# Performance work log

Hardware: AMD Instinct MI355X
Metric: run time of the kernel (lower is better)

Reference implementation:

```python
import jax, jax.numpy as jnp
import numpy as np

B, CIN, HALF, H, W = 4, 3, 32, 512, 512
K_MODE, PAD_MODE, N_LEVELS = 11, 5, 17  # 11x11 mode window, reflect pad 5, round(x*255/16) in 0..16
SLOPE, EPS = 0.01, 1e-5


def _leaky(x):
    return jnp.where(x > 0, x, SLOPE * x)


def _bn(x, g, b):
    # BatchNorm2d in training mode: batch statistics over (B,H,W), biased var
    m = x.mean(axis=(0, 2, 3), keepdims=True)
    v = x.var(axis=(0, 2, 3), keepdims=True)
    return (x - m) * jax.lax.rsqrt(v + EPS) * g[None, :, None, None] + b[None, :, None, None]


def _mode_pool(x):
    # quantize to 17 discrete levels, then sliding-window histogram mode (fused
    # equivalent of unfold + torch.mode; argmax first-hit == smallest tied value)
    k = jnp.clip(jnp.round(x * (255.0 / 16.0)), 0, N_LEVELS - 1).astype(jnp.int32)
    kp = jnp.pad(k, ((0, 0), (0, 0), (PAD_MODE, PAD_MODE), (PAD_MODE, PAD_MODE)), mode='reflect')
    onehot = (kp[..., None] == jnp.arange(N_LEVELS, dtype=jnp.int32)).astype(jnp.float32)
    counts = jax.lax.reduce_window(onehot, 0.0, jax.lax.add,
                                   (1, 1, K_MODE, K_MODE, 1), (1, 1, 1, 1, 1), 'VALID')
    mode_k = jnp.argmax(counts, axis=-1)  # [B,C,H,W]
    return mode_k.astype(jnp.float32) * (16.0 / 256.0)


def _nearest(x, Ho, Wo):
    # torch interpolate(mode='nearest'): src = floor(dst * in/out)
    hi, wi = x.shape[2], x.shape[3]
    ri = (jnp.arange(Ho) * hi) // Ho
    ci = (jnp.arange(Wo) * wi) // Wo
    return x[:, :, ri][:, :, :, ci]


def _forward(x, w1, b1, w2, b2, bn1_g, bn1_b, w3, b3, bn2_g, bn2_b,
             k_down, k_w, bnw_g, bnw_b, k_h, bnh_g, bnh_b):
    xm = _mode_pool(x)  # [B,CIN,H,W]
    # prepare: 1x1 conv -> LeakyReLU -> 1x1 conv -> BN -> LeakyReLU -> depthwise 1x1 -> BN -> LeakyReLU
    h = _leaky(jnp.einsum('bchw,oc->bohw', xm, w1) + b1[None, :, None, None])
    h = jnp.einsum('bchw,oc->bohw', h, w2) + b2[None, :, None, None]
    h = _leaky(_bn(h, bn1_g, bn1_b))
    h = h * w3[None, :, None, None] + b3[None, :, None, None]  # groups=half 1x1 conv
    h = _leaky(_bn(h, bn2_g, bn2_b))
    Bs, half, Ho, Wo = h.shape
    score = jnp.zeros((Bs, 2 * half, Ho, Wo), jnp.float32)
    d = h
    while min(d.shape[2], d.shape[3]) >= 3:  # static pyramid: 512->171->57->19->7->3->1
        d = jax.lax.conv_general_dilated(d, k_down, (3, 3), ((1, 1), (1, 1)),
                                         dimension_numbers=('NCHW', 'OIHW', 'NCHW'),
                                         feature_group_count=half)
        z = _nearest(d, Ho, Wo)
        wbr = _leaky(_bn(z * k_w[None, :, None, None], bnw_g, bnw_b))  # width branch (SharedConv k=1, no bias)
        hbr = _leaky(_bn(z * k_h[None, :, None, None], bnh_g, bnh_b))  # height branch
        # stack(dim=1).reshape => width channels first, then height channels
        score = score + jnp.concatenate([wbr, hbr], axis=1)
    return score


def setup_inputs():
    key = jax.random.key(0)
    ks = jax.random.split(key, 8)
    x = jax.random.uniform(ks[0], (B, CIN, H, W), dtype=jnp.float32)
    s1, s2 = 1.0 / np.sqrt(CIN), 1.0 / np.sqrt(2 * CIN)
    return {
        'x': x,
        'w1': jax.random.uniform(ks[1], (2 * CIN, CIN), jnp.float32, -s1, s1),
        'b1': jax.random.uniform(ks[2], (2 * CIN,), jnp.float32, -s1, s1),
        'w2': jax.random.uniform(ks[3], (HALF, 2 * CIN), jnp.float32, -s2, s2),
        'b2': jax.random.uniform(ks[4], (HALF,), jnp.float32, -s2, s2),
        'bn1_g': jnp.ones((HALF,), jnp.float32),
        'bn1_b': jnp.zeros((HALF,), jnp.float32),
        'w3': jax.random.uniform(ks[5], (HALF,), jnp.float32, -1.0, 1.0),
        'b3': jax.random.uniform(ks[6], (HALF,), jnp.float32, -1.0, 1.0),
        'bn2_g': jnp.ones((HALF,), jnp.float32),
        'bn2_b': jnp.zeros((HALF,), jnp.float32),
        'k_down': jnp.full((HALF, 1, 3, 3), 0.5, jnp.float32),  # SharedConv init
        'k_w': jnp.full((HALF,), 0.5, jnp.float32),
        'bnw_g': jnp.ones((HALF,), jnp.float32),
        'bnw_b': jnp.zeros((HALF,), jnp.float32),
        'k_h': jnp.full((HALF,), 0.5, jnp.float32),
        'bnh_g': jnp.ones((HALF,), jnp.float32),
        'bnh_b': jnp.zeros((HALF,), jnp.float32),
    }


def reference(x, w1, b1, w2, b2, bn1_g, bn1_b, w3, b3, bn2_g, bn2_b,
              k_down, k_w, bnw_g, bnw_b, k_h, bnh_g, bnh_b):
    return _forward(x, w1, b1, w2, b2, bn1_g, bn1_b, w3, b3, bn2_g, bn2_b,
                    k_down, k_w, bnw_g, bnw_b, k_h, bnh_g, bnh_b)
```

## Files before the change

kernel.cpp:

```cpp
#include <hip/hip_runtime.h>

#define HH 512
#define WW 512
#define HW 262144
#define NPIX 1048576
#define NPIXF 1048576.0f

typedef float f4 __attribute__((ext_vector_type(4)));

__device__ __forceinline__ float leaky(float v) { return v > 0.f ? v : 0.01f * v; }

__device__ __forceinline__ float repw(int i, int s) {
    return (float)(((i + 1) * 512 + s - 1) / s - (i * 512 + s - 1) / s);
}

__device__ __forceinline__ void hins(unsigned long long& h0, unsigned long long& h1,
                                     unsigned& c16, int val) {
    unsigned long long inc = 1ull << ((val & 7) * 8);
    h0 += (val < 8) ? inc : 0;
    h1 += (val >= 8 && val < 16) ? inc : 0;
    c16 += (unsigned)(val >> 4);
}
__device__ __forceinline__ void hrem(unsigned long long& h0, unsigned long long& h1,
                                     unsigned& c16, int val) {
    unsigned long long inc = 1ull << ((val & 7) * 8);
    h0 -= (val < 8) ? inc : 0;
    h1 -= (val >= 8 && val < 16) ? inc : 0;
    c16 -= (unsigned)(val >> 4);
}

__global__ __launch_bounds__(256) void mode_kernel(const float* __restrict__ x,
                                                   unsigned char* __restrict__ modeq,
                                                   const float* __restrict__ w1,
                                                   const float* __restrict__ b1,
                                                   unsigned* __restrict__ partial,
                                                   float* __restrict__ mpart) {
    __shared__ unsigned char q[26 * 272];
    __shared__ unsigned ch[2][267 * 5];
    __shared__ unsigned lh[4913];
    __shared__ float mred[27][4];
    const int t = threadIdx.x;
    for (int i = t; i < 4913; i += 256) lh[i] = 0;
    const int tc0 = blockIdx.x * 256;
    const int tr0 = blockIdx.y * 16;
    const int bb = blockIdx.z;
    unsigned rp[3][4];
    for (int p = 0; p < 3; ++p) {
        const float* xp = x + (size_t)(bb * 3 + p) * HW;
        for (int idx = t; idx < 26 * 266; idx += 256) {
            int r = idx / 266;
            int cc = idx - r * 266;
            int gr = tr0 + r - 5; gr = gr < 0 ? -gr : (gr > 511 ? 1022 - gr : gr);
            int gc = tc0 + cc - 5; gc = gc < 0 ? -gc : (gc > 511 ? 1022 - gc : gc);
            float v = rintf(xp[gr * WW + gc] * 15.9375f);
            v = fminf(fmaxf(v, 0.f), 16.f);
            q[r * 272 + cc] = (unsigned char)(int)v;
        }
        unsigned long long A0 = 0, A1 = 0; unsigned A2 = 0;
        unsigned long long B0 = 0, B1 = 0; unsigned B2 = 0;
        unsigned wkw[4] = {0u, 0u, 0u, 0u};
        __syncthreads();
        for (int r = 0; r < 16; ++r) {
            if (r == 0) {
                #pragma unroll
                for (int v = 0; v < 11; ++v) {
                    hins(A0, A1, A2, q[v * 272 + t]);
                    if (t < 10) hins(B0, B1, B2, q[v * 272 + 256 + t]);
                }
            } else {
                hrem(A0, A1, A2, q[(r - 1) * 272 + t]);
                hins(A0, A1, A2, q[(r + 10) * 272 + t]);
                if (t < 10) {
                    hrem(B0, B1, B2, q[(r - 1) * 272 + 256 + t]);
                    hins(B0, B1, B2, q[(r + 10) * 272 + 256 + t]);
                }
            }
            unsigned* cb = ch[r & 1];
            cb[t * 5 + 0] = (unsigned)A0;
            cb[t * 5 + 1] = (unsigned)(A0 >> 32);
            cb[t * 5 + 2] = (unsigned)A1;
            cb[t * 5 + 3] = (unsigned)(A1 >> 32);
            cb[t * 5 + 4] = A2;
            if (t < 10) {
                cb[(256 + t) * 5 + 0] = (unsigned)B0;
                cb[(256 + t) * 5 + 1] = (unsigned)(B0 >> 32);
                cb[(256 + t) * 5 + 2] = (unsigned)B1;
                cb[(256 + t) * 5 + 3] = (unsigned)(B1 >> 32);
                cb[(256 + t) * 5 + 4] = B2;
            }
            __syncthreads();
            unsigned long long H0 = 0, H1 = 0; unsigned C = 0;
            #pragma unroll
            for (int v = 0; v < 11; ++v) {
                const unsigned* pk = &cb[(t + v) * 5];
                H0 += (unsigned long long)pk[0] | ((unsigned long long)pk[1] << 32);
                H1 += (unsigned long long)pk[2] | ((unsigned long long)pk[3] << 32);
                C += pk[4];
            }
            unsigned m = 0;
            #pragma unroll
            for (int i = 0; i < 8; ++i) {
                unsigned cnt = (unsigned)(H0 >> (8 * i)) & 0xFFu;
                unsigned val = (cnt << 8) | (unsigned)(16 - i);
                m = m > val ? m : val;
            }
            #pragma unroll
            for (int i = 8; i < 16; ++i) {
                unsigned cnt = (unsigned)(H1 >> (8 * (i - 8))) & 0xFFu;
                unsigned val = (cnt << 8) | (unsigned)(16 - i);
                m = m > val ? m : val;
            }
            unsigned val16 = (C << 8);
            m = m > val16 ? m : val16;
            int k = 16 - (int)(m & 0xFFu);
            wkw[r >> 2] |= (unsigned)k << ((r & 3) * 8);
            modeq[(size_t)(bb * 3 + p) * HW + (size_t)(tr0 + r) * WW + tc0 + t] = (unsigned char)k;
        }
        rp[p][0] = wkw[0]; rp[p][1] = wkw[1]; rp[p][2] = wkw[2]; rp[p][3] = wkw[3];
    }
    #pragma unroll
    for (int r = 0; r < 16; ++r) {
        int sh = (r & 3) * 8;
        int k0 = (rp[0][r >> 2] >> sh) & 0xFF;
        int k1 = (rp[1][r >> 2] >> sh) & 0xFF;
        int k2 = (rp[2][r >> 2] >> sh) & 0xFF;
        atomicAdd(&lh[k0 + 17 * k1 + 289 * k2], 1u);
    }
    __syncthreads();
    const int blk = blockIdx.x + 2 * (blockIdx.y + 32 * blockIdx.z);
    for (int i = t; i < 4913; i += 256) partial[i * 256 + blk] = lh[i];
    float w1r[18], b1r[6];
    #pragma unroll
    for (int k = 0; k < 18; ++k) w1r[k] = w1[k];
    #pragma unroll
    for (int o = 0; o < 6; ++o) b1r[o] = b1[o];
    float M[27];
    #pragma unroll
    for (int i = 0; i < 27; ++i) M[i] = 0.f;
    for (int bin = t; bin < 4913; bin += 256) {
        float cnt = (float)lh[bin];
        int k0 = bin % 17;
        int r = bin / 17;
        int k1 = r % 17;
        int k2 = r / 17;
        float xm0 = k0 * 0.0625f, xm1 = k1 * 0.0625f, xm2 = k2 * 0.0625f;
        float t1[6];
        #pragma unroll
        for (int o = 0; o < 6; ++o)
            t1[o] = leaky(xm0 * w1r[o * 3] + xm1 * w1r[o * 3 + 1] + xm2 * w1r[o * 3 + 2] + b1r[o]);
        #pragma unroll
        for (int o = 0; o < 6; ++o) M[o] += cnt * t1[o];
        int ii = 6;
        #pragma unroll
        for (int j = 0; j < 6; ++j)
            #pragma unroll
            for (int k = j; k < 6; ++k) { M[ii] += cnt * t1[j] * t1[k]; ++ii; }
    }
    int wv = t >> 6;
    #pragma unroll
    for (int i = 0; i < 27; ++i) {
        float v = M[i];
        #pragma unroll
        for (int off = 32; off >= 1; off >>= 1) v += __shfl_xor(v, off);
        if ((t & 63) == 0) mred[i][wv] = v;
    }
    __syncthreads();
    if (t < 27)
        mpart[blk * 27 + t] = mred[t][0] + mred[t][1] + mred[t][2] + mred[t][3];
}

__global__ __launch_bounds__(1024) void solveA_kernel(const float* __restrict__ mpart,
                                                      const float* __restrict__ w2,
                                                      const float* __restrict__ b2,
                                                      const float* __restrict__ g1,
                                                      const float* __restrict__ bb1,
                                                      float* __restrict__ p1) {
    __shared__ float red[32][32];
    __shared__ float mom[27];
    int t = threadIdx.x;
    int i = t & 31, g = t >> 5;
    float s = 0.f;
    if (i < 27) {
        #pragma unroll
        for (int j = 0; j < 8; ++j) s += mpart[(g + 32 * j) * 27 + i];
    }
    red[g][i] = s;
    __syncthreads();
    if (t < 27) {
        float v = 0.f;
        #pragma unroll
        for (int gg = 0; gg < 32; ++gg) v += red[gg][t];
        mom[t] = v;
    }
    __syncthreads();
    if (t < 32) {
        int c = t;
        float w2r[6];
        #pragma unroll
        for (int k = 0; k < 6; ++k) w2r[k] = w2[c * 6 + k];
        float b2c = b2[c];
        float wm1 = 0.f;
        #pragma unroll
        for (int k = 0; k < 6; ++k) wm1 += w2r[k] * mom[k];
        float q = 0.f;
        int ii = 6;
        #pragma unroll
        for (int j = 0; j < 6; ++j)
            #pragma unroll
            for (int k = j; k < 6; ++k) {
                float f = w2r[j] * w2r[k] * mom[ii];
                q += (j == k) ? f : 2.f * f;
                ++ii;
            }
        float mean = b2c + wm1 / NPIXF;
        float ex2 = b2c * b2c + 2.f * b2c * (wm1 / NPIXF) + q / NPIXF;
        float var = ex2 - mean * mean;
        float a = g1[c] * rsqrtf(var + 1e-5f);
        p1[c] = a;
        p1[32 + c] = bb1[c] - mean * a;
    }
}

__global__ __launch_bounds__(256) void solveB_kernel(const unsigned* __restrict__ partial,
                                                     const float* __restrict__ w1,
                                                     const float* __restrict__ b1,
                                                     const float* __restrict__ w2,
                                                     const float* __restrict__ b2,
                                                     const float* __restrict__ p1,
                                                     float* __restrict__ tpart) {
    __shared__ float rs[8][32], rq[8][32];
    int c = threadIdx.x & 31;
    int sub = threadIdx.x >> 5;
    float w1r[18], b1r[6];
    #pragma unroll
    for (int k = 0; k < 18; ++k) w1r[k] = w1[k];
    #pragma unroll
    for (int o = 0; o < 6; ++o) b1r[o] = b1[o];
    float w2r[6];
    #pragma unroll
    for (int k = 0; k < 6; ++k) w2r[k] = w2[c * 6 + k];
    float b2c = b2[c];
    float a1 = p1[c], c1 = p1[32 + c];
    float sm = 0.f, sq = 0.f;
    for (int bin = blockIdx.x + 32 * sub; bin < 4913; bin += 256) {
        unsigned cs = 0;
        const unsigned* pb = partial + (size_t)bin * 256;
        #pragma unroll
        for (int j = 0; j < 8; ++j) cs += pb[c + 32 * j];
        #pragma unroll
        for (int off = 16; off >= 1; off >>= 1) cs += __shfl_xor((int)cs, off);
        float cnt = (float)cs;
        int k0 = bin % 17;
        int r = bin / 17;
        int k1 = r % 17;
        int k2 = r / 17;
        float xm0 = k0 * 0.0625f, xm1 = k1 * 0.0625f, xm2 = k2 * 0.0625f;
        float t1[6];
        #pragma unroll
        for (int o = 0; o < 6; ++o)
            t1[o] = leaky(xm0 * w1r[o * 3] + xm1 * w1r[o * 3 + 1] + xm2 * w1r[o * 3 + 2] + b1r[o]);
        float h2 = b2c;
        #pragma unroll
        for (int k = 0; k < 6; ++k) h2 += w2r[k] * t1[k];
        float t = leaky(a1 * h2 + c1);
        sm += cnt * t;
        sq += cnt * t * t;
    }
    rs[sub][c] = sm; rq[sub][c] = sq;
    __syncthreads();
    if (threadIdx.x < 32) {
        float s = 0.f, qq = 0.f;
        #pragma unroll
        for (int g = 0; g < 8; ++g) { s += rs[g][threadIdx.x]; qq += rq[g][threadIdx.x]; }
        tpart[blockIdx.x * 64 + threadIdx.x] = s;
        tpart[blockIdx.x * 64 + 32 + threadIdx.x] = qq;
    }
}

__global__ void fin2_kernel(const float* __restrict__ tpart, const float* __restrict__ w3,
                            const float* __restrict__ b3, const float* __restrict__ g,
                            const float* __restrict__ bb, float* __restrict__ p2) {
    int c = threadIdx.x;
    float s = 0.f, qq = 0.f;
    #pragma unroll
    for (int k = 0; k < 32; ++k) { s += tpart[k * 64 + c]; qq += tpart[k * 64 + 32 + c]; }
    float mt = s / NPIXF;
    float vt = qq / NPIXF - mt * mt;
    float m2 = w3[c] * mt + b3[c];
    float v2 = w3[c] * w3[c] * vt;
    float a = g[c] * rsqrtf(v2 + 1e-5f);
    p2[c] = a;
    p2[32 + c] = bb[c] - m2 * a;
}

__global__ __launch_bounds__(64) void d1_kernel(const unsigned char* __restrict__ modeq,
                                                const float* __restrict__ w1,
                                                const float* __restrict__ b1,
                                                const float* __restrict__ w2,
                                                const float* __restrict__ b2,
                                                const float* __restrict__ w3,
                                                const float* __restrict__ b3,
                                                const float* __restrict__ p1,
                                                const float* __restrict__ p2,
                                                const float* __restrict__ kd,
                                                float* __restrict__ d1) {
    int j = blockIdx.x * 64 + threadIdx.x;
    if (j >= 171) return;
    int i = blockIdx.y;
    int b = blockIdx.z;
    float acc[32];
    #pragma unroll
    for (int c = 0; c < 32; ++c) acc[c] = 0.f;
    const unsigned char* mp = modeq + (size_t)b * 3 * HW;
    #pragma unroll
    for (int u = 0; u < 3; ++u) {
        int r = 3 * i - 1 + u;
        if (r < 0 || r > 511) continue;
        #pragma unroll
        for (int v = 0; v < 3; ++v) {
            int col = 3 * j - 1 + v;
            if (col < 0 || col > 511) continue;
            int off = r * WW + col;
            float xm0 = mp[off] * 0.0625f, xm1 = mp[off + HW] * 0.0625f, xm2 = mp[off + 2 * HW] * 0.0625f;
            float t1[6];
            #pragma unroll
            for (int o = 0; o < 6; ++o)
                t1[o] = leaky(xm0 * w1[o * 3] + xm1 * w1[o * 3 + 1] + xm2 * w1[o * 3 + 2] + b1[o]);
            #pragma unroll
            for (int c = 0; c < 32; ++c) {
                float h2 = b2[c];
                #pragma unroll
                for (int k = 0; k < 6; ++k) h2 += w2[c * 6 + k] * t1[k];
                float t = leaky(h2 * p1[c] + p1[32 + c]);
                float uu = t * w3[c] + b3[c];
                float hv = leaky(uu * p2[c] + p2[32 + c]);
                acc[c] += hv * kd[c * 9 + u * 3 + v];
            }
        }
    }
    size_t base = ((size_t)(b * 32) * 171 + i) * 171 + j;
    #pragma unroll
    for (int c = 0; c < 32; ++c) d1[base + (size_t)c * 29241] = acc[c];
}

__device__ __forceinline__ void red_store(float sm, float sq, float* rsc, float* ps) {
    #pragma unroll
    for (int off = 32; off >= 1; off >>= 1) {
        sm += __shfl_xor(sm, off);
        sq += __shfl_xor(sq, off);
    }
    __syncthreads();
    int wv = threadIdx.x >> 6;
    if ((threadIdx.x & 63) == 0) { rsc[wv] = sm; rsc[8 + wv] = sq; }
    __syncthreads();
    if (threadIdx.x == 0) {
        ps[0] = rsc[0] + rsc[1] + rsc[2] + rsc[3];
        ps[1] = rsc[8] + rsc[9] + rsc[10] + rsc[11];
    }
}

__device__ __forceinline__ void lvl(const float* src, int sin, float* dstL,
                                    float* dstG, int sout, const float* kreg,
                                    float* rsc, float* ps) {
    float sm = 0.f, sq = 0.f;
    int n = sout * sout;
    for (int i = threadIdx.x; i < n; i += 256) {
        int oi = i / sout, oj = i - oi * sout;
        float acc = 0.f;
        #pragma unroll
        for (int u = 0; u < 3; ++u) {
            int r = 3 * oi - 1 + u;
            if ((unsigned)r >= (unsigned)sin) continue;
            #pragma unroll
            for (int v = 0; v < 3; ++v) {
                int cc = 3 * oj - 1 + v;
                if ((unsigned)cc >= (unsigned)sin) continue;
                acc += src[r * sin + cc] * kreg[u * 3 + v];
            }
        }
        dstG[i] = acc;
        if (dstL) dstL[i] = acc;
        float w = repw(oi, sout) * repw(oj, sout);
        sm += w * acc;
        sq += w * acc * acc;
    }
    red_store(sm, sq, rsc, ps);
}

__global__ __launch_bounds__(256) void pyramid_kernel(const float* __restrict__ d1,
                                                      float* __restrict__ d2,
                                                      float* __restrict__ d3,
                                                      float* __restrict__ d4,
                                                      float* __restrict__ d5,
                                                      float* __restrict__ d6,
                                                      const float* __restrict__ kd,
                                                      float* __restrict__ pstats) {
    __shared__ float buf2[3249];
    __shared__ float buf3[361];
    __shared__ float buf4[49];
    __shared__ float buf5[9];
    __shared__ float rsc[16];
    int bc = blockIdx.x;
    int c = bc & 31;
    float kreg[9];
    #pragma unroll
    for (int qq = 0; qq < 9; ++qq) kreg[qq] = kd[c * 9 + qq];
    float* ps = pstats + (size_t)bc * 12;
    const float* s1 = d1 + (size_t)bc * 29241;
    float sm = 0.f, sq = 0.f;
    for (int i = threadIdx.x; i < 29241; i += 256) {
        int oi = i / 171, oj = i - oi * 171;
        float w = repw(oi, 171) * repw(oj, 171);
        float v = s1[i];
        sm += w * v;
        sq += w * v * v;
    }
    red_store(sm, sq, rsc, ps + 0);
    lvl(s1, 171, buf2, d2 + (size_t)bc * 3249, 57, kreg, rsc, ps + 2);
    lvl(buf2, 57, buf3, d3 + (size_t)bc * 361, 19, kreg, rsc, ps + 4);
    lvl(buf3, 19, buf4, d4 + (size_t)bc * 49, 7, kreg, rsc, ps + 6);
    lvl(buf4, 7, buf5, d5 + (size_t)bc * 9, 3, kreg, rsc, ps + 8);
    lvl(buf5, 3, nullptr, d6 + bc, 1, kreg, rsc, ps + 10);
}

__global__ void fin3_kernel(const float* __restrict__ pstats, const float* __restrict__ kw,
                            const float* __restrict__ gw, const float* __restrict__ bw,
                            const float* __restrict__ kh, const float* __restrict__ gh,
                            const float* __restrict__ bh, float* __restrict__ lp) {
    int t = threadIdx.x;
    if (t >= 192) return;
    int l = t >> 5, c = t & 31;
    float sm = 0.f, sq = 0.f;
    #pragma unroll
    for (int b = 0; b < 4; ++b) {
        const float* ps = pstats + (size_t)(b * 32 + c) * 12 + 2 * l;
        sm += ps[0];
        sq += ps[1];
    }
    float mz = sm / NPIXF;
    float vz = sq / NPIXF - mz * mz;
    float kwc = kw[c];
    float aw = gw[c] * rsqrtf(kwc * kwc * vz + 1e-5f);
    float khc = kh[c];
    float ah = gh[c] * rsqrtf(khc * khc * vz + 1e-5f);
    float* o = lp + (size_t)(l * 32 + c) * 4;
    o[0] = kwc * aw;
    o[1] = bw[c] - kwc * mz * aw;
    o[2] = khc * ah;
    o[3] = bh[c] - khc * mz * ah;
}

__global__ __launch_bounds__(256) void final_kernel(const float* __restrict__ d1,
                                                    const float* __restrict__ d2,
                                                    const float* __restrict__ d3,
                                                    const float* __restrict__ d4,
                                                    const float* __restrict__ d5,
                                                    const float* __restrict__ d6,
                                                    const float* __restrict__ lp,
                                                    float* __restrict__ out) {
    int idx = blockIdx.x * 256 + threadIdx.x;
    int w4 = (idx & 127) << 2;
    int h = (idx >> 7) & 511;
    int c = (idx >> 16) & 31;
    int b = idx >> 21;
    const float* ds[6] = {d1, d2, d3, d4, d5, d6};
    const int ss[6] = {171, 57, 19, 7, 3, 1};
    float accw[4] = {0.f, 0.f, 0.f, 0.f};
    float acch[4] = {0.f, 0.f, 0.f, 0.f};
    #pragma unroll
    for (int l = 0; l < 6; ++l) {
        int s = ss[l];
        int sh = (h * s) >> 9;
        const float* base = ds[l] + ((size_t)(b * 32 + c) * s + sh) * s;
        const float* a = lp + (size_t)(l * 32 + c) * 4;
        float a0 = a[0], a1 = a[1], a2 = a[2], a3 = a[3];
        #pragma unroll
        for (int k = 0; k < 4; ++k) {
            int sw = ((w4 + k) * s) >> 9;
            float val = base[sw];
            accw[k] += leaky(val * a0 + a1);
            acch[k] += leaky(val * a2 + a3);
        }
    }
    size_t o = (((size_t)(b * 64 + c)) << 18) + ((size_t)h << 9) + w4;
    f4 vw = {accw[0], accw[1], accw[2], accw[3]};
    f4 vh = {acch[0], acch[1], acch[2], acch[3]};
    __builtin_nontemporal_store(vw, (f4*)(out + o));
    __builtin_nontemporal_store(vh, (f4*)(out + o + (((size_t)32) << 18)));
}

extern "C" void kernel_launch(void* const* d_in, const int* in_sizes, int n_in,
                              void* d_out, int out_size, void* d_ws, size_t ws_size,
                              hipStream_t stream) {
    const float* x     = (const float*)d_in[0];
    const float* w1    = (const float*)d_in[1];
    const float* b1    = (const float*)d_in[2];
    const float* w2    = (const float*)d_in[3];
    const float* b2    = (const float*)d_in[4];
    const float* bn1g  = (const float*)d_in[5];
    const float* bn1b  = (const float*)d_in[6];
    const float* w3    = (const float*)d_in[7];
    const float* b3    = (const float*)d_in[8];
    const float* bn2g  = (const float*)d_in[9];
    const float* bn2b  = (const float*)d_in[10];
    const float* kd    = (const float*)d_in[11];
    const float* kw    = (const float*)d_in[12];
    const float* bnwg  = (const float*)d_in[13];
    const float* bnwb  = (const float*)d_in[14];
    const float* kh    = (const float*)d_in[15];
    const float* bnhg  = (const float*)d_in[16];
    const float* bnhb  = (const float*)d_in[17];
    float* out = (float*)d_out;

    char* ws = (char*)d_ws;
    unsigned char* modeq = (unsigned char*)ws;
    float* mpart  = (float*)(ws + 3145728);
    float* tpart  = (float*)(ws + 3145728 + 27648);
    float* pstats = (float*)(ws + 3145728 + 27648 + 8192);
    float* p1 = (float*)(ws + 3187712);
    float* p2 = p1 + 64;
    float* lp = p2 + 64;
    unsigned* partial = (unsigned*)(ws + 3191296);
    float* d1 = (float*)(ws + 3191296 + 5030912);
    float* d2 = d1 + 3742848;
    float* d3 = d2 + 415872;
    float* d4 = d3 + 46208;
    float* d5 = d4 + 6272;
    float* d6 = d5 + 1152;

    mode_kernel<<<dim3(2, 32, 4), 256, 0, stream>>>(x, modeq, w1, b1, partial, mpart);
    solveA_kernel<<<1, 1024, 0, stream>>>(mpart, w2, b2, bn1g, bn1b, p1);
    solveB_kernel<<<32, 256, 0, stream>>>(partial, w1, b1, w2, b2, p1, tpart);
    fin2_kernel<<<1, 32, 0, stream>>>(tpart, w3, b3, bn2g, bn2b, p2);
    d1_kernel<<<dim3(3, 171, 4), 64, 0, stream>>>(modeq, w1, b1, w2, b2, w3, b3, p1, p2, kd, d1);
    pyramid_kernel<<<128, 256, 0, stream>>>(d1, d2, d3, d4, d5, d6, kd, pstats);
    fin3_kernel<<<1, 192, 0, stream>>>(pstats, kw, bnwg, bnwb, kh, bnhg, bnhb, lp);
    final_kernel<<<32768, 256, 0, stream>>>(d1, d2, d3, d4, d5, d6, lp, out);
}
```

Baseline: 504.4 us.

## Split mode pooling per plane, move joint histogram to separate kernel, fuse tiny solvers

The mode kernel now runs one block per (tile, plane) across 12 planes instead of looping over 3 channels inside each block, giving three times more blocks. The joint 3-channel histogram and moment accumulation move into a new hist_kernel that rereads the quantized mode bytes. solveA is folded into solveB, with every block recomputing the BN1 parameters, and fin3 is folded into final_kernel, with each block recomputing its per-channel coefficients. This removes two launches and gives the mode pass more parallelism, at the cost of an extra read of modeq and redundant small computations.

```diff
diff --git a/kernel.cpp b/kernel.cpp
--- a/kernel.cpp
+++ b/kernel.cpp
@@ -30,105 +30,114 @@
 }
 
 __global__ __launch_bounds__(256) void mode_kernel(const float* __restrict__ x,
-                                                   unsigned char* __restrict__ modeq,
+                                                   unsigned char* __restrict__ modeq) {
+    __shared__ unsigned char q[26 * 272];
+    __shared__ unsigned ch[2][267 * 5];
+    const int plane = blockIdx.z;
+    const int tc0 = blockIdx.x * 256;
+    const int tr0 = blockIdx.y * 16;
+    const float* xp = x + (size_t)plane * HW;
+    for (int idx = threadIdx.x; idx < 26 * 266; idx += 256) {
+        int r = idx / 266;
+        int cc = idx - r * 266;
+        int gr = tr0 + r - 5; gr = gr < 0 ? -gr : (gr > 511 ? 1022 - gr : gr);
+        int gc = tc0 + cc - 5; gc = gc < 0 ? -gc : (gc > 511 ? 1022 - gc : gc);
+        float v = rintf(xp[gr * WW + gc] * 15.9375f);
+        v = fminf(fmaxf(v, 0.f), 16.f);
+        q[r * 272 + cc] = (unsigned char)(int)v;
+    }
+    const int t = threadIdx.x;
+    unsigned long long A0 = 0, A1 = 0; unsigned A2 = 0;
+    unsigned long long B0 = 0, B1 = 0; unsigned B2 = 0;
+    __syncthreads();
+    for (int r = 0; r < 16; ++r) {
+        if (r == 0) {
+            #pragma unroll
+            for (int v = 0; v < 11; ++v) {
+                hins(A0, A1, A2, q[v * 272 + t]);
+                if (t < 10) hins(B0, B1, B2, q[v * 272 + 256 + t]);
+            }
+        } else {
+            hrem(A0, A1, A2, q[(r - 1) * 272 + t]);
+            hins(A0, A1, A2, q[(r + 10) * 272 + t]);
+            if (t < 10) {
+                hrem(B0, B1, B2, q[(r - 1) * 272 + 256 + t]);
+                hins(B0, B1, B2, q[(r + 10) * 272 + 256 + t]);
+            }
+        }
+        unsigned* cb = ch[r & 1];
+        cb[t * 5 + 0] = (unsigned)A0;
+        cb[t * 5 + 1] = (unsigned)(A0 >> 32);
+        cb[t * 5 + 2] = (unsigned)A1;
+        cb[t * 5 + 3] = (unsigned)(A1 >> 32);
+        cb[t * 5 + 4] = A2;
+        if (t < 10) {
+            cb[(256 + t) * 5 + 0] = (unsigned)B0;
+            cb[(256 + t) * 5 + 1] = (unsigned)(B0 >> 32);
+            cb[(256 + t) * 5 + 2] = (unsigned)B1;
+            cb[(256 + t) * 5 + 3] = (unsigned)(B1 >> 32);
+            cb[(256 + t) * 5 + 4] = B2;
+        }
+        __syncthreads();
+        unsigned long long H0 = 0, H1 = 0; unsigned C = 0;
+        #pragma unroll
+        for (int v = 0; v < 11; ++v) {
+            const unsigned* p = &cb[(t + v) * 5];
+            H0 += (unsigned long long)p[0] | ((unsigned long long)p[1] << 32);
+            H1 += (unsigned long long)p[2] | ((unsigned long long)p[3] << 32);
+            C += p[4];
+        }
+        unsigned m = 0;
+        #pragma unroll
+        for (int i = 0; i < 8; ++i) {
+            unsigned cnt = (unsigned)(H0 >> (8 * i)) & 0xFFu;
+            unsigned val = (cnt << 8) | (unsigned)(16 - i);
+            m = m > val ? m : val;
+        }
+        #pragma unroll
+        for (int i = 8; i < 16; ++i) {
+            unsigned cnt = (unsigned)(H1 >> (8 * (i - 8))) & 0xFFu;
+            unsigned val = (cnt << 8) | (unsigned)(16 - i);
+            m = m > val ? m : val;
+        }
+        unsigned val16 = (C << 8);
+        m = m > val16 ? m : val16;
+        int k = 16 - (int)(m & 0xFFu);
+        modeq[(size_t)plane * HW + (size_t)(tr0 + r) * WW + tc0 + t] = (unsigned char)k;
+    }
+}
+
+__global__ __launch_bounds__(256) void hist_kernel(const unsigned char* __restrict__ modeq,
                                                    const float* __restrict__ w1,
                                                    const float* __restrict__ b1,
                                                    unsigned* __restrict__ partial,
                                                    float* __restrict__ mpart) {
-    __shared__ unsigned char q[26 * 272];
-    __shared__ unsigned ch[2][267 * 5];
     __shared__ unsigned lh[4913];
     __shared__ float mred[27][4];
-    const int t = threadIdx.x;
-    for (int i = t; i < 4913; i += 256) lh[i] = 0;
-    const int tc0 = blockIdx.x * 256;
-    const int tr0 = blockIdx.y * 16;
-    const int bb = blockIdx.z;
-    unsigned rp[3][4];
-    for (int p = 0; p < 3; ++p) {
-        const float* xp = x + (size_t)(bb * 3 + p) * HW;
-        for (int idx = t; idx < 26 * 266; idx += 256) {
-            int r = idx / 266;
-            int cc = idx - r * 266;
-            int gr = tr0 + r - 5; gr = gr < 0 ? -gr : (gr > 511 ? 1022 - gr : gr);
-            int gc = tc0 + cc - 5; gc = gc < 0 ? -gc : (gc > 511 ? 1022 - gc : gc);
-            float v = rintf(xp[gr * WW + gc] * 15.9375f);
-            v = fminf(fmaxf(v, 0.f), 16.f);
-            q[r * 272 + cc] = (unsigned char)(int)v;
-        }
-        unsigned long long A0 = 0, A1 = 0; unsigned A2 = 0;
-        unsigned long long B0 = 0, B1 = 0; unsigned B2 = 0;
-        unsigned wkw[4] = {0u, 0u, 0u, 0u};
-        __syncthreads();
-        for (int r = 0; r < 16; ++r) {
-            if (r == 0) {
-                #pragma unroll
-                for (int v = 0; v < 11; ++v) {
-                    hins(A0, A1, A2, q[v * 272 + t]);
-                    if (t < 10) hins(B0, B1, B2, q[v * 272 + 256 + t]);
-                }
-            } else {
-                hrem(A0, A1, A2, q[(r - 1) * 272 + t]);
-                hins(A0, A1, A2, q[(r + 10) * 272 + t]);
-                if (t < 10) {
-                    hrem(B0, B1, B2, q[(r - 1) * 272 + 256 + t]);
-                    hins(B0, B1, B2, q[(r + 10) * 272 + 256 + t]);
-                }
-            }
-            unsigned* cb = ch[r & 1];
-            cb[t * 5 + 0] = (unsigned)A0;
-            cb[t * 5 + 1] = (unsigned)(A0 >> 32);
-            cb[t * 5 + 2] = (unsigned)A1;
-            cb[t * 5 + 3] = (unsigned)(A1 >> 32);
-            cb[t * 5 + 4] = A2;
-            if (t < 10) {
-                cb[(256 + t) * 5 + 0] = (unsigned)B0;
-                cb[(256 + t) * 5 + 1] = (unsigned)(B0 >> 32);
-                cb[(256 + t) * 5 + 2] = (unsigned)B1;
-                cb[(256 + t) * 5 + 3] = (unsigned)(B1 >> 32);
-                cb[(256 + t) * 5 + 4] = B2;
-            }
-            __syncthreads();
-            unsigned long long H0 = 0, H1 = 0; unsigned C = 0;
-            #pragma unroll
-            for (int v = 0; v < 11; ++v) {
-                const unsigned* pk = &cb[(t + v) * 5];
-                H0 += (unsigned long long)pk[0] | ((unsigned long long)pk[1] << 32);
-                H1 += (unsigned long long)pk[2] | ((unsigned long long)pk[3] << 32);
-                C += pk[4];
-            }
-            unsigned m = 0;
-            #pragma unroll
-            for (int i = 0; i < 8; ++i) {
-                unsigned cnt = (unsigned)(H0 >> (8 * i)) & 0xFFu;
-                unsigned val = (cnt << 8) | (unsigned)(16 - i);
-                m = m > val ? m : val;
-            }
-            #pragma unroll
-            for (int i = 8; i < 16; ++i) {
-                unsigned cnt = (unsigned)(H1 >> (8 * (i - 8))) & 0xFFu;
-                unsigned val = (cnt << 8) | (unsigned)(16 - i);
-                m = m > val ? m : val;
-            }
-            unsigned val16 = (C << 8);
-            m = m > val16 ? m : val16;
-            int k = 16 - (int)(m & 0xFFu);
-            wkw[r >> 2] |= (unsigned)k << ((r & 3) * 8);
-            modeq[(size_t)(bb * 3 + p) * HW + (size_t)(tr0 + r) * WW + tc0 + t] = (unsigned char)k;
-        }
-        rp[p][0] = wkw[0]; rp[p][1] = wkw[1]; rp[p][2] = wkw[2]; rp[p][3] = wkw[3];
-    }
-    #pragma unroll
-    for (int r = 0; r < 16; ++r) {
-        int sh = (r & 3) * 8;
-        int k0 = (rp[0][r >> 2] >> sh) & 0xFF;
-        int k1 = (rp[1][r >> 2] >> sh) & 0xFF;
-        int k2 = (rp[2][r >> 2] >> sh) & 0xFF;
-        atomicAdd(&lh[k0 + 17 * k1 + 289 * k2], 1u);
-    }
-    __syncthreads();
-    const int blk = blockIdx.x + 2 * (blockIdx.y + 32 * blockIdx.z);
-    for (int i = t; i < 4913; i += 256) partial[i * 256 + blk] = lh[i];
+    for (int i = threadIdx.x; i < 4913; i += 256) lh[i] = 0;
+    __syncthreads();
+    int base = blockIdx.x * 8192;
+    int b = base >> 18;
+    int hw0 = base & (HW - 1);
+    const unsigned char* mp = modeq + (size_t)b * 3 * HW;
+    #pragma unroll
+    for (int j = 0; j < 8; ++j) {
+        int g = threadIdx.x + 256 * j;
+        int hw = hw0 + g * 4;
+        unsigned u0 = *(const unsigned*)(mp + hw);
+        unsigned u1 = *(const unsigned*)(mp + hw + HW);
+        unsigned u2 = *(const unsigned*)(mp + hw + 2 * HW);
+        #pragma unroll
+        for (int k = 0; k < 4; ++k) {
+            int k0 = (u0 >> (8 * k)) & 0xFF;
+            int k1 = (u1 >> (8 * k)) & 0xFF;
+            int k2 = (u2 >> (8 * k)) & 0xFF;
+            atomicAdd(&lh[k0 + 17 * k1 + 289 * k2], 1u);
+        }
+    }
+    __syncthreads();
+    unsigned* pp = partial + blockIdx.x * 4913;
+    for (int i = threadIdx.x; i < 4913; i += 256) pp[i] = lh[i];
     float w1r[18], b1r[6];
     #pragma unroll
     for (int k = 0; k < 18; ++k) w1r[k] = w1[k];
@@ -137,7 +146,7 @@
     float M[27];
     #pragma unroll
     for (int i = 0; i < 27; ++i) M[i] = 0.f;
-    for (int bin = t; bin < 4913; bin += 256) {
+    for (int bin = threadIdx.x; bin < 4913; bin += 256) {
         float cnt = (float)lh[bin];
         int k0 = bin % 17;
         int r = bin / 17;
@@ -156,49 +165,59 @@
             #pragma unroll
             for (int k = j; k < 6; ++k) { M[ii] += cnt * t1[j] * t1[k]; ++ii; }
     }
-    int wv = t >> 6;
+    int wv = threadIdx.x >> 6;
     #pragma unroll
     for (int i = 0; i < 27; ++i) {
         float v = M[i];
         #pragma unroll
         for (int off = 32; off >= 1; off >>= 1) v += __shfl_xor(v, off);
-        if ((t & 63) == 0) mred[i][wv] = v;
-    }
-    __syncthreads();
-    if (t < 27)
-        mpart[blk * 27 + t] = mred[t][0] + mred[t][1] + mred[t][2] + mred[t][3];
-}
-
-__global__ __launch_bounds__(1024) void solveA_kernel(const float* __restrict__ mpart,
+        if ((threadIdx.x & 63) == 0) mred[i][wv] = v;
+    }
+    __syncthreads();
+    if (threadIdx.x < 27)
+        mpart[blockIdx.x * 27 + threadIdx.x] =
+            mred[threadIdx.x][0] + mred[threadIdx.x][1] +
+            mred[threadIdx.x][2] + mred[threadIdx.x][3];
+}
+
+__global__ __launch_bounds__(256) void solveBF_kernel(const float* __restrict__ mpart,
+                                                      const unsigned* __restrict__ partial,
+                                                      const float* __restrict__ w1,
+                                                      const float* __restrict__ b1,
                                                       const float* __restrict__ w2,
                                                       const float* __restrict__ b2,
                                                       const float* __restrict__ g1,
                                                       const float* __restrict__ bb1,
-                                                      float* __restrict__ p1) {
-    __shared__ float red[32][32];
+                                                      float* __restrict__ p1g,
+                                                      float* __restrict__ tpart) {
+    __shared__ float red[8][32];
     __shared__ float mom[27];
-    int t = threadIdx.x;
-    int i = t & 31, g = t >> 5;
-    float s = 0.f;
-    if (i < 27) {
-        #pragma unroll
-        for (int j = 0; j < 8; ++j) s += mpart[(g + 32 * j) * 27 + i];
-    }
-    red[g][i] = s;
+    __shared__ float a1s[32], c1s[32];
+    __shared__ float rs[8][32], rq[8][32];
+    const int t = threadIdx.x;
+    const int c = t & 31;
+    const int sub = t >> 5;
+    {
+        float s = 0.f;
+        if (c < 27) {
+            #pragma unroll
+            for (int j = 0; j < 16; ++j) s += mpart[(sub * 16 + j) * 27 + c];
+        }
+        red[sub][c] = s;
+    }
     __syncthreads();
     if (t < 27) {
         float v = 0.f;
         #pragma unroll
-        for (int gg = 0; gg < 32; ++gg) v += red[gg][t];
+        for (int g = 0; g < 8; ++g) v += red[g][t];
         mom[t] = v;
     }
     __syncthreads();
     if (t < 32) {
-        int c = t;
         float w2r[6];
         #pragma unroll
-        for (int k = 0; k < 6; ++k) w2r[k] = w2[c * 6 + k];
-        float b2c = b2[c];
+        for (int k = 0; k < 6; ++k) w2r[k] = w2[t * 6 + k];
+        float b2c = b2[t];
         float wm1 = 0.f;
         #pragma unroll
         for (int k = 0; k < 6; ++k) wm1 += w2r[k] * mom[k];
@@ -215,22 +234,12 @@
         float mean = b2c + wm1 / NPIXF;
         float ex2 = b2c * b2c + 2.f * b2c * (wm1 / NPIXF) + q / NPIXF;
         float var = ex2 - mean * mean;
-        float a = g1[c] * rsqrtf(var + 1e-5f);
-        p1[c] = a;
-        p1[32 + c] = bb1[c] - mean * a;
-    }
-}
-
-__global__ __launch_bounds__(256) void solveB_kernel(const unsigned* __restrict__ partial,
-                                                     const float* __restrict__ w1,
-                                                     const float* __restrict__ b1,
-                                                     const float* __restrict__ w2,
-                                                     const float* __restrict__ b2,
-                                                     const float* __restrict__ p1,
-                                                     float* __restrict__ tpart) {
-    __shared__ float rs[8][32], rq[8][32];
-    int c = threadIdx.x & 31;
-    int sub = threadIdx.x >> 5;
+        float a = g1[t] * rsqrtf(var + 1e-5f);
+        a1s[t] = a;
+        c1s[t] = bb1[t] - mean * a;
+        if (blockIdx.x == 0) { p1g[t] = a; p1g[32 + t] = c1s[t]; }
+    }
+    __syncthreads();
     float w1r[18], b1r[6];
     #pragma unroll
     for (int k = 0; k < 18; ++k) w1r[k] = w1[k];
@@ -240,13 +249,13 @@
     #pragma unroll
     for (int k = 0; k < 6; ++k) w2r[k] = w2[c * 6 + k];
     float b2c = b2[c];
-    float a1 = p1[c], c1 = p1[32 + c];
+    float a1 = a1s[c], c1 = c1s[c];
     float sm = 0.f, sq = 0.f;
     for (int bin = blockIdx.x + 32 * sub; bin < 4913; bin += 256) {
         unsigned cs = 0;
-        const unsigned* pb = partial + (size_t)bin * 256;
-        #pragma unroll
-        for (int j = 0; j < 8; ++j) cs += pb[c + 32 * j];
+        const unsigned* pb = partial + bin;
+        #pragma unroll
+        for (int j = 0; j < 4; ++j) cs += pb[(size_t)(c + 32 * j) * 4913];
         #pragma unroll
         for (int off = 16; off >= 1; off >>= 1) cs += __shfl_xor((int)cs, off);
         float cnt = (float)cs;
@@ -262,18 +271,18 @@
         float h2 = b2c;
         #pragma unroll
         for (int k = 0; k < 6; ++k) h2 += w2r[k] * t1[k];
-        float t = leaky(a1 * h2 + c1);
-        sm += cnt * t;
-        sq += cnt * t * t;
+        float tt = leaky(a1 * h2 + c1);
+        sm += cnt * tt;
+        sq += cnt * tt * tt;
     }
     rs[sub][c] = sm; rq[sub][c] = sq;
     __syncthreads();
-    if (threadIdx.x < 32) {
+    if (t < 32) {
         float s = 0.f, qq = 0.f;
         #pragma unroll
-        for (int g = 0; g < 8; ++g) { s += rs[g][threadIdx.x]; qq += rq[g][threadIdx.x]; }
-        tpart[blockIdx.x * 64 + threadIdx.x] = s;
-        tpart[blockIdx.x * 64 + 32 + threadIdx.x] = qq;
+        for (int g = 0; g < 8; ++g) { s += rs[g][t]; qq += rq[g][t]; }
+        tpart[blockIdx.x * 64 + t] = s;
+        tpart[blockIdx.x * 64 + 32 + t] = qq;
     }
 }
 
@@ -423,46 +432,47 @@
     lvl(buf5, 3, nullptr, d6 + bc, 1, kreg, rsc, ps + 10);
 }
 
-__global__ void fin3_kernel(const float* __restrict__ pstats, const float* __restrict__ kw,
-                            const float* __restrict__ gw, const float* __restrict__ bw,
-                            const float* __restrict__ kh, const float* __restrict__ gh,
-                            const float* __restrict__ bh, float* __restrict__ lp) {
-    int t = threadIdx.x;
-    if (t >= 192) return;
-    int l = t >> 5, c = t & 31;
-    float sm = 0.f, sq = 0.f;
-    #pragma unroll
-    for (int b = 0; b < 4; ++b) {
-        const float* ps = pstats + (size_t)(b * 32 + c) * 12 + 2 * l;
-        sm += ps[0];
-        sq += ps[1];
-    }
-    float mz = sm / NPIXF;
-    float vz = sq / NPIXF - mz * mz;
-    float kwc = kw[c];
-    float aw = gw[c] * rsqrtf(kwc * kwc * vz + 1e-5f);
-    float khc = kh[c];
-    float ah = gh[c] * rsqrtf(khc * khc * vz + 1e-5f);
-    float* o = lp + (size_t)(l * 32 + c) * 4;
-    o[0] = kwc * aw;
-    o[1] = bw[c] - kwc * mz * aw;
-    o[2] = khc * ah;
-    o[3] = bh[c] - khc * mz * ah;
-}
-
 __global__ __launch_bounds__(256) void final_kernel(const float* __restrict__ d1,
                                                     const float* __restrict__ d2,
                                                     const float* __restrict__ d3,
                                                     const float* __restrict__ d4,
                                                     const float* __restrict__ d5,
                                                     const float* __restrict__ d6,
-                                                    const float* __restrict__ lp,
+                                                    const float* __restrict__ pstats,
+                                                    const float* __restrict__ kw,
+                                                    const float* __restrict__ gw,
+                                                    const float* __restrict__ bw,
+                                                    const float* __restrict__ kh,
+                                                    const float* __restrict__ gh,
+                                                    const float* __restrict__ bh,
                                                     float* __restrict__ out) {
+    __shared__ float la[6][4];
     int idx = blockIdx.x * 256 + threadIdx.x;
+    int c = (idx >> 16) & 31;
+    int b = idx >> 21;
+    if (threadIdx.x < 6) {
+        int l = threadIdx.x;
+        float sm = 0.f, sq = 0.f;
+        #pragma unroll
+        for (int b4 = 0; b4 < 4; ++b4) {
+            const float* ps = pstats + (size_t)(b4 * 32 + c) * 12 + 2 * l;
+            sm += ps[0];
+            sq += ps[1];
+        }
+        float mz = sm / NPIXF;
+        float vz = sq / NPIXF - mz * mz;
+        float kwc = kw[c];
+        float aw = gw[c] * rsqrtf(kwc * kwc * vz + 1e-5f);
+        float khc = kh[c];
+        float ah = gh[c] * rsqrtf(khc * khc * vz + 1e-5f);
+        la[l][0] = kwc * aw;
+        la[l][1] = bw[c] - kwc * mz * aw;
+        la[l][2] = khc * ah;
+        la[l][3] = bh[c] - khc * mz * ah;
+    }
+    __syncthreads();
     int w4 = (idx & 127) << 2;
     int h = (idx >> 7) & 511;
-    int c = (idx >> 16) & 31;
-    int b = idx >> 21;
     const float* ds[6] = {d1, d2, d3, d4, d5, d6};
     const int ss[6] = {171, 57, 19, 7, 3, 1};
     float accw[4] = {0.f, 0.f, 0.f, 0.f};
@@ -472,8 +482,7 @@
         int s = ss[l];
         int sh = (h * s) >> 9;
         const float* base = ds[l] + ((size_t)(b * 32 + c) * s + sh) * s;
-        const float* a = lp + (size_t)(l * 32 + c) * 4;
-        float a0 = a[0], a1 = a[1], a2 = a[2], a3 = a[3];
+        float a0 = la[l][0], a1 = la[l][1], a2 = la[l][2], a3 = la[l][3];
         #pragma unroll
         for (int k = 0; k < 4; ++k) {
             int sw = ((w4 + k) * s) >> 9;
@@ -515,25 +524,25 @@
     char* ws = (char*)d_ws;
     unsigned char* modeq = (unsigned char*)ws;
     float* mpart  = (float*)(ws + 3145728);
-    float* tpart  = (float*)(ws + 3145728 + 27648);
-    float* pstats = (float*)(ws + 3145728 + 27648 + 8192);
-    float* p1 = (float*)(ws + 3187712);
+    float* tpart  = (float*)(ws + 3145728 + 13824);
+    float* pstats = (float*)(ws + 3145728 + 13824 + 8192);
+    float* p1 = (float*)(ws + 3174400);
     float* p2 = p1 + 64;
-    float* lp = p2 + 64;
-    unsigned* partial = (unsigned*)(ws + 3191296);
-    float* d1 = (float*)(ws + 3191296 + 5030912);
+    unsigned* partial = (unsigned*)(ws + 3174912);
+    float* d1 = (float*)(ws + 3174912 + 2515456);
     float* d2 = d1 + 3742848;
     float* d3 = d2 + 415872;
     float* d4 = d3 + 46208;
     float* d5 = d4 + 6272;
     float* d6 = d5 + 1152;
 
-    mode_kernel<<<dim3(2, 32, 4), 256, 0, stream>>>(x, modeq, w1, b1, partial, mpart);
-    solveA_kernel<<<1, 1024, 0, stream>>>(mpart, w2, b2, bn1g, bn1b, p1);
-    solveB_kernel<<<32, 256, 0, stream>>>(partial, w1, b1, w2, b2, p1, tpart);
+    mode_kernel<<<dim3(2, 32, 12), 256, 0, stream>>>(x, modeq);
+    hist_kernel<<<128, 256, 0, stream>>>(modeq, w1, b1, partial, mpart);
+    solveBF_kernel<<<32, 256, 0, stream>>>(mpart, partial, w1, b1, w2, b2,
+                                           bn1g, bn1b, p1, tpart);
     fin2_kernel<<<1, 32, 0, stream>>>(tpart, w3, b3, bn2g, bn2b, p2);
     d1_kernel<<<dim3(3, 171, 4), 64, 0, stream>>>(modeq, w1, b1, w2, b2, w3, b3, p1, p2, kd, d1);
     pyramid_kernel<<<128, 256, 0, stream>>>(d1, d2, d3, d4, d5, d6, kd, pstats);
-    fin3_kernel<<<1, 192, 0, stream>>>(pstats, kw, bnwg, bnwb, kh, bnhg, bnhb, lp);
-    final_kernel<<<32768, 256, 0, stream>>>(d1, d2, d3, d4, d5, d6, lp, out);
-}
+    final_kernel<<<32768, 256, 0, stream>>>(d1, d2, d3, d4, d5, d6, pstats,
+                                            kw, bnwg, bnwb, kh, bnhg, bnhb, out);
+}
```

After: 482.7 us. 4.3% less time.
